# Optimization experiments

Hardware: AMD Instinct MI355X
Metric: run time of the kernel (lower is better)

## Reference

```python
import jax, jax.numpy as jnp
import numpy as np

B, T_DEC, S_ENC, D = 4, 128, 1024, 512
UNITS = 128


def setup_inputs() -> dict:
    key = jax.random.key(0)
    ks = jax.random.split(key, 5)
    dec = jax.random.normal(ks[0], (B, T_DEC, D), dtype=jnp.float32)
    enc = jax.random.normal(ks[1], (B, S_ENC, D), dtype=jnp.float32)
    # Glorot-ish scaled dense params
    W1 = jax.random.normal(ks[2], (D, UNITS), dtype=jnp.float32) / np.sqrt(D)
    b1 = jnp.zeros((UNITS,), dtype=jnp.float32)
    W2 = jax.random.normal(ks[3], (D, UNITS), dtype=jnp.float32) / np.sqrt(D)
    b2 = jnp.zeros((UNITS,), dtype=jnp.float32)
    v = jax.random.normal(ks[4], (UNITS,), dtype=jnp.float32) / np.sqrt(UNITS)
    v_b = jnp.zeros((1,), dtype=jnp.float32)
    return {"decoder_output": dec, "encoder_output": enc,
            "W1": W1, "b1": b1, "W2": W2, "b2": b2, "v": v, "v_b": v_b}


def reference(decoder_output, encoder_output, W1, b1, W2, b2, v, v_b):
    # Hoist the loop-invariant encoder projection (original recomputes it per step).
    w_enc = encoder_output @ W1 + b1            # [B, S, U]
    w_dec = decoder_output @ W2 + b2            # [B, T, U]
    # score[b,t,s] = v . tanh(w_enc[b,s] + w_dec[b,t]) + v_bias
    feat = jnp.tanh(w_enc[:, None, :, :] + w_dec[:, :, None, :])  # [B, T, S, U]
    scores = jnp.einsum('btsu,u->bts', feat, v) + v_b[0]          # [B, T, S]
    attention_weights = jax.nn.softmax(scores, axis=-1)           # [B, T, S]
    context_vector = jnp.einsum('bts,bsd->btd', attention_weights, encoder_output)
    return (context_vector, attention_weights)
```

## Files before the change

kernel.cpp:

```cpp
#include <hip/hip_runtime.h>
#include <math.h>

#define NB 4
#define TD 128
#define SE 1024
#define DD 512
#define UN 128
#define KSPLIT 4

__device__ __forceinline__ float exp2_raw(float x) {
  float r;
  asm("v_exp_f32 %0, %1" : "=v"(r) : "v"(x));
  return r;
}

__global__ __launch_bounds__(512, 2) void k_proj(const float* __restrict__ enc,
                                                 const float* __restrict__ dec,
                                                 const float* __restrict__ W1,
                                                 const float* __restrict__ b1,
                                                 const float* __restrict__ W2,
                                                 const float* __restrict__ b2,
                                                 float* __restrict__ wencT,
                                                 float* __restrict__ wdec) {
  __shared__ __align__(16) float At[16 * DD];
  __shared__ float red[KSPLIT][16][129];

  const int tx = threadIdx.x;
  const int rb = blockIdx.x;
  const bool is_enc = rb < 256;
  const int row_base = rb * 16;
  const float* __restrict__ src = is_enc
      ? (enc + (size_t)row_base * DD)
      : (dec + (size_t)(row_base - NB * SE) * DD);
  const float* __restrict__ W = is_enc ? W1 : W2;
  const float* __restrict__ bias = is_enc ? b1 : b2;
  const float K2 = 2.88539008f;

#pragma unroll
  for (int i = 0; i < 4; ++i) {
    const int idx = (i * 512 + tx) * 4;
    *(float4*)&At[idx] = *(const float4*)(src + idx);
  }
  __syncthreads();

  const int u2 = (tx & 63) * 2;
  const int wave = tx >> 6;
  const int ks = wave & 3;
  const int rh = wave >> 2;
  const int kb = ks * 128;
  const float* __restrict__ Wp = W + (size_t)kb * UN + u2;

  float acc[8][2] = {};
  for (int k = 0; k < 128; k += 4) {
    float4 a[8];
#pragma unroll
    for (int r = 0; r < 8; ++r)
      a[r] = *(const float4*)&At[(rh * 8 + r) * DD + kb + k];
#pragma unroll
    for (int j = 0; j < 4; ++j) {
      const float2 w = *(const float2*)(Wp + (size_t)(k + j) * UN);
#pragma unroll
      for (int r = 0; r < 8; ++r) {
        const float arj = ((const float*)&a[r])[j];
        acc[r][0] = fmaf(arj, w.x, acc[r][0]);
        acc[r][1] = fmaf(arj, w.y, acc[r][1]);
      }
    }
  }

#pragma unroll
  for (int r = 0; r < 8; ++r) {
    red[ks][rh * 8 + r][u2]     = acc[r][0];
    red[ks][rh * 8 + r][u2 + 1] = acc[r][1];
  }
  __syncthreads();

  const int u = tx >> 2;
  const int rq = (tx & 3) * 4;
  const float bu = bias[u];
  if (is_enc) {
    float o[4];
#pragma unroll
    for (int j = 0; j < 4; ++j) {
      const int row = rq + j;
      const float s = (red[0][row][u] + red[1][row][u]) +
                      (red[2][row][u] + red[3][row][u]);
      o[j] = exp2_raw(K2 * (s + bu));
    }
    const int b = row_base >> 10;
    const int s0 = row_base & 1023;
    *(float4*)(wencT + (size_t)(b * UN + u) * SE + s0 + rq) =
        make_float4(o[0], o[1], o[2], o[3]);
  } else {
    const int rb0 = row_base - NB * SE;
#pragma unroll
    for (int j = 0; j < 4; ++j) {
      const int row = rq + j;
      const float s = (red[0][row][u] + red[1][row][u]) +
                      (red[2][row][u] + red[3][row][u]);
      wdec[(size_t)(rb0 + row) * UN + u] = K2 * (s + bu);
    }
  }
}

__global__ __launch_bounds__(1024, 1) void k_score(const float* __restrict__ wdec,
                                                   const float* __restrict__ v,
                                                   const float* __restrict__ wencT,
                                                   float* __restrict__ attn) {
  __shared__ __align__(16) float wdE[2][UN];
  __shared__ __align__(16) float nv2[UN];
  __shared__ __align__(16) float parts[4][2][SE];
  __shared__ float redM[2][4], redS[2][4];

  const int wg = blockIdx.x;
  const int b = wg >> 6;
  const int t0 = (wg & 63) * 2;
  const int bt0 = b * TD + t0;
  const int tx = threadIdx.x;

  if (tx < 2 * UN) {
    const int tt = tx >> 7, u = tx & 127;
    wdE[tt][u] = exp2_raw(wdec[(size_t)(bt0 + tt) * UN + u]);
    if (tx < UN) nv2[tx] = -2.0f * v[tx];
  }
  __syncthreads();

  const int sq = tx & 255;
  const int uq = tx >> 8;
  const float* wp = wencT + (size_t)(b * UN + uq * 32) * SE + sq * 4;

  float a0[4] = {}, a1[4] = {};
#pragma unroll 2
  for (int ui4 = 0; ui4 < 32; ui4 += 4) {
    const int u0 = uq * 32 + ui4;
    const float4 nv = *(const float4*)&nv2[u0];
    const float4 E0v = *(const float4*)&wdE[0][u0];
    const float4 E1v = *(const float4*)&wdE[1][u0];
#pragma unroll
    for (int m = 0; m < 4; ++m) {
      const float4 ew = *(const float4*)(wp + (size_t)(ui4 + m) * SE);
      const float nvu = ((const float*)&nv)[m];
      const float E0 = ((const float*)&E0v)[m];
      const float E1 = ((const float*)&E1v)[m];
#pragma unroll
      for (int j = 0; j < 4; ++j) {
        const float e = ((const float*)&ew)[j];
        const float r0 = __builtin_amdgcn_rcpf(fmaf(e, E0, 1.0f));
        a0[j] = fmaf(nvu, r0, a0[j]);
        const float r1 = __builtin_amdgcn_rcpf(fmaf(e, E1, 1.0f));
        a1[j] = fmaf(nvu, r1, a1[j]);
      }
    }
  }
  *(float4*)&parts[uq][0][sq * 4] = make_float4(a0[0], a0[1], a0[2], a0[3]);
  *(float4*)&parts[uq][1][sq * 4] = make_float4(a1[0], a1[1], a1[2], a1[3]);
  __syncthreads();

  float sc[4], pv[4];
  const int tt = tx >> 8;
  const int q = tx & 255;
  if (tx < 512) {
    const float4 g0 = *(const float4*)&parts[0][tt][q * 4];
    const float4 g1 = *(const float4*)&parts[1][tt][q * 4];
    const float4 g2 = *(const float4*)&parts[2][tt][q * 4];
    const float4 g3 = *(const float4*)&parts[3][tt][q * 4];
    sc[0] = (g0.x + g1.x) + (g2.x + g3.x);
    sc[1] = (g0.y + g1.y) + (g2.y + g3.y);
    sc[2] = (g0.z + g1.z) + (g2.z + g3.z);
    sc[3] = (g0.w + g1.w) + (g2.w + g3.w);
    float m = fmaxf(fmaxf(sc[0], sc[1]), fmaxf(sc[2], sc[3]));
#pragma unroll
    for (int off = 32; off; off >>= 1) m = fmaxf(m, __shfl_xor(m, off));
    if ((tx & 63) == 0) redM[tt][(tx >> 6) & 3] = m;
  }
  __syncthreads();
  if (tx < 512) {
    const float m = fmaxf(fmaxf(redM[tt][0], redM[tt][1]),
                          fmaxf(redM[tt][2], redM[tt][3]));
    float s = 0.f;
#pragma unroll
    for (int j = 0; j < 4; ++j) { pv[j] = __expf(sc[j] - m); s += pv[j]; }
#pragma unroll
    for (int off = 32; off; off >>= 1) s += __shfl_xor(s, off);
    if ((tx & 63) == 0) redS[tt][(tx >> 6) & 3] = s;
  }
  __syncthreads();
  if (tx < 512) {
    const float s = (redS[tt][0] + redS[tt][1]) + (redS[tt][2] + redS[tt][3]);
    const float rinv = 1.0f / s;
    float* arow = attn + (size_t)(bt0 + tt) * SE + q * 4;
    *(float4*)arow = make_float4(pv[0] * rinv, pv[1] * rinv, pv[2] * rinv, pv[3] * rinv);
  }
}

__global__ __launch_bounds__(1024, 1) void k_ctx(const float* __restrict__ attn,
                                                 const float* __restrict__ enc,
                                                 float* __restrict__ ctx) {
  __shared__ __align__(16) float at[8][SE];
  __shared__ __align__(16) float red[16][8][128];

  const int wg = blockIdx.x;
  const int dt = wg & 3;
  const int tg = (wg >> 2) & 15;
  const int b = wg >> 6;
  const int tx = threadIdx.x;

#pragma unroll
  for (int i = 0; i < 2; ++i) {
    const int idx = i * 1024 + tx;
    const int row = idx >> 8;
    const int c = (idx & 255) * 4;
    *(float4*)&at[row][c] =
        *(const float4*)(attn + (size_t)(b * TD + tg * 8 + row) * SE + c);
  }
  __syncthreads();

  const int w = tx >> 6;
  const int dp = (tx & 63) * 2;
  const int sbeg = w * 64;
  const float* ep = enc + ((size_t)b * SE + sbeg) * DD + dt * 128 + dp;

  float2 acc[8] = {};
  for (int s = 0; s < 64; s += 4) {
    float4 av[8];
#pragma unroll
    for (int t = 0; t < 8; ++t)
      av[t] = *(const float4*)&at[t][sbeg + s];
#pragma unroll
    for (int j = 0; j < 4; ++j) {
      const float2 ev = *(const float2*)(ep + (size_t)(s + j) * DD);
#pragma unroll
      for (int t = 0; t < 8; ++t) {
        const float a = ((const float*)&av[t])[j];
        acc[t].x = fmaf(a, ev.x, acc[t].x);
        acc[t].y = fmaf(a, ev.y, acc[t].y);
      }
    }
  }
#pragma unroll
  for (int t = 0; t < 8; ++t)
    *(float2*)&red[w][t][dp] = acc[t];
  __syncthreads();

  const int t = tx >> 7;
  const int d = tx & 127;
  float o = 0.f;
#pragma unroll
  for (int q = 0; q < 16; ++q) o += red[q][t][d];
  ctx[(size_t)(b * TD + tg * 8 + t) * DD + dt * 128 + d] = o;
}

extern "C" void kernel_launch(void* const* d_in, const int* in_sizes, int n_in,
                              void* d_out, int out_size, void* d_ws, size_t ws_size,
                              hipStream_t stream) {
  const float* dec = (const float*)d_in[0];
  const float* enc = (const float*)d_in[1];
  const float* W1  = (const float*)d_in[2];
  const float* b1  = (const float*)d_in[3];
  const float* W2  = (const float*)d_in[4];
  const float* b2  = (const float*)d_in[5];
  const float* v   = (const float*)d_in[6];

  float* ctx  = (float*)d_out;
  float* attn = (float*)d_out + (size_t)NB * TD * DD;

  float* ws    = (float*)d_ws;
  float* wencT = ws;
  float* wdec  = wencT + (size_t)NB * UN * SE;

  hipLaunchKernelGGL(k_proj, dim3(288), dim3(512), 0, stream,
                     enc, dec, W1, b1, W2, b2, wencT, wdec);
  hipLaunchKernelGGL(k_score, dim3(256), dim3(1024), 0, stream,
                     wdec, v, wencT, attn);
  hipLaunchKernelGGL(k_ctx, dim3(256), dim3(1024), 0, stream, attn, enc, ctx);
}
```

Measured before the change: 45.25 us.

## Reduce score partials across lanes with shuffles instead of shared memory

```diff
diff --git a/kernel.cpp b/kernel.cpp
--- a/kernel.cpp
+++ b/kernel.cpp
@@ -107,10 +107,9 @@
                                                    const float* __restrict__ v,
                                                    const float* __restrict__ wencT,
                                                    float* __restrict__ attn) {
-  __shared__ __align__(16) float wdE[2][UN];
-  __shared__ __align__(16) float nv2[UN];
-  __shared__ __align__(16) float parts[4][2][SE];
-  __shared__ float redM[2][4], redS[2][4];
+  __shared__ __align__(16) float wdEr[2][4][132];
+  __shared__ __align__(16) float nv2r[4][132];
+  __shared__ float redM[2][16], redS[2][16];
 
   const int wg = blockIdx.x;
   const int b = wg >> 6;
@@ -120,22 +119,28 @@
 
   if (tx < 2 * UN) {
     const int tt = tx >> 7, u = tx & 127;
-    wdE[tt][u] = exp2_raw(wdec[(size_t)(bt0 + tt) * UN + u]);
-    if (tx < UN) nv2[tx] = -2.0f * v[tx];
-  }
-  __syncthreads();
-
-  const int sq = tx & 255;
-  const int uq = tx >> 8;
+    const float e = exp2_raw(wdec[(size_t)(bt0 + tt) * UN + u]);
+#pragma unroll
+    for (int c = 0; c < 4; ++c) wdEr[tt][c][u] = e;
+    if (tx < UN) {
+      const float nv = -2.0f * v[tx];
+#pragma unroll
+      for (int c = 0; c < 4; ++c) nv2r[c][tx] = nv;
+    }
+  }
+  __syncthreads();
+
+  const int sq = tx >> 2;
+  const int uq = tx & 3;
   const float* wp = wencT + (size_t)(b * UN + uq * 32) * SE + sq * 4;
 
   float a0[4] = {}, a1[4] = {};
 #pragma unroll 2
   for (int ui4 = 0; ui4 < 32; ui4 += 4) {
     const int u0 = uq * 32 + ui4;
-    const float4 nv = *(const float4*)&nv2[u0];
-    const float4 E0v = *(const float4*)&wdE[0][u0];
-    const float4 E1v = *(const float4*)&wdE[1][u0];
+    const float4 nv = *(const float4*)&nv2r[uq][u0];
+    const float4 E0v = *(const float4*)&wdEr[0][uq][u0];
+    const float4 E1v = *(const float4*)&wdEr[1][uq][u0];
 #pragma unroll
     for (int m = 0; m < 4; ++m) {
       const float4 ew = *(const float4*)(wp + (size_t)(ui4 + m) * SE);
@@ -152,44 +157,56 @@
       }
     }
   }
-  *(float4*)&parts[uq][0][sq * 4] = make_float4(a0[0], a0[1], a0[2], a0[3]);
-  *(float4*)&parts[uq][1][sq * 4] = make_float4(a1[0], a1[1], a1[2], a1[3]);
-  __syncthreads();
-
-  float sc[4], pv[4];
-  const int tt = tx >> 8;
-  const int q = tx & 255;
-  if (tx < 512) {
-    const float4 g0 = *(const float4*)&parts[0][tt][q * 4];
-    const float4 g1 = *(const float4*)&parts[1][tt][q * 4];
-    const float4 g2 = *(const float4*)&parts[2][tt][q * 4];
-    const float4 g3 = *(const float4*)&parts[3][tt][q * 4];
-    sc[0] = (g0.x + g1.x) + (g2.x + g3.x);
-    sc[1] = (g0.y + g1.y) + (g2.y + g3.y);
-    sc[2] = (g0.z + g1.z) + (g2.z + g3.z);
-    sc[3] = (g0.w + g1.w) + (g2.w + g3.w);
-    float m = fmaxf(fmaxf(sc[0], sc[1]), fmaxf(sc[2], sc[3]));
-#pragma unroll
-    for (int off = 32; off; off >>= 1) m = fmaxf(m, __shfl_xor(m, off));
-    if ((tx & 63) == 0) redM[tt][(tx >> 6) & 3] = m;
-  }
-  __syncthreads();
-  if (tx < 512) {
-    const float m = fmaxf(fmaxf(redM[tt][0], redM[tt][1]),
-                          fmaxf(redM[tt][2], redM[tt][3]));
-    float s = 0.f;
-#pragma unroll
-    for (int j = 0; j < 4; ++j) { pv[j] = __expf(sc[j] - m); s += pv[j]; }
-#pragma unroll
-    for (int off = 32; off; off >>= 1) s += __shfl_xor(s, off);
-    if ((tx & 63) == 0) redS[tt][(tx >> 6) & 3] = s;
-  }
-  __syncthreads();
-  if (tx < 512) {
-    const float s = (redS[tt][0] + redS[tt][1]) + (redS[tt][2] + redS[tt][3]);
-    const float rinv = 1.0f / s;
-    float* arow = attn + (size_t)(bt0 + tt) * SE + q * 4;
-    *(float4*)arow = make_float4(pv[0] * rinv, pv[1] * rinv, pv[2] * rinv, pv[3] * rinv);
+
+#pragma unroll
+  for (int j = 0; j < 4; ++j) {
+    a0[j] += __shfl_xor(a0[j], 1); a0[j] += __shfl_xor(a0[j], 2);
+    a1[j] += __shfl_xor(a1[j], 1); a1[j] += __shfl_xor(a1[j], 2);
+  }
+
+  float m0 = fmaxf(fmaxf(a0[0], a0[1]), fmaxf(a0[2], a0[3]));
+  float m1 = fmaxf(fmaxf(a1[0], a1[1]), fmaxf(a1[2], a1[3]));
+#pragma unroll
+  for (int off = 4; off <= 32; off <<= 1) {
+    m0 = fmaxf(m0, __shfl_xor(m0, off));
+    m1 = fmaxf(m1, __shfl_xor(m1, off));
+  }
+  const int wv = tx >> 6;
+  if ((tx & 63) == 0) { redM[0][wv] = m0; redM[1][wv] = m1; }
+  __syncthreads();
+  m0 = redM[0][0]; m1 = redM[1][0];
+#pragma unroll
+  for (int q = 1; q < 16; ++q) {
+    m0 = fmaxf(m0, redM[0][q]);
+    m1 = fmaxf(m1, redM[1][q]);
+  }
+
+  float p0[4], p1[4];
+  float s0 = 0.f, s1 = 0.f;
+#pragma unroll
+  for (int j = 0; j < 4; ++j) {
+    p0[j] = __expf(a0[j] - m0); s0 += p0[j];
+    p1[j] = __expf(a1[j] - m1); s1 += p1[j];
+  }
+#pragma unroll
+  for (int off = 4; off <= 32; off <<= 1) {
+    s0 += __shfl_xor(s0, off);
+    s1 += __shfl_xor(s1, off);
+  }
+  if ((tx & 63) == 0) { redS[0][wv] = s0; redS[1][wv] = s1; }
+  __syncthreads();
+  s0 = 0.f; s1 = 0.f;
+#pragma unroll
+  for (int q = 0; q < 16; ++q) { s0 += redS[0][q]; s1 += redS[1][q]; }
+  const float r0 = 1.0f / s0;
+  const float r1 = 1.0f / s1;
+
+  if (uq == 0) {
+    float* arow0 = attn + (size_t)bt0 * SE + sq * 4;
+    *(float4*)arow0 =
+        make_float4(p0[0] * r0, p0[1] * r0, p0[2] * r0, p0[3] * r0);
+    *(float4*)(arow0 + SE) =
+        make_float4(p1[0] * r1, p1[1] * r1, p1[2] * r1, p1[3] * r1);
   }
 }
 
```

New measurement: 52.14 us. 1.15x slower.

## Restructure score kernel to one decoder step per 512-thread block

Applied to the files above, without the earlier changes.

```diff
diff --git a/kernel.cpp b/kernel.cpp
--- a/kernel.cpp
+++ b/kernel.cpp
@@ -103,93 +103,82 @@
   }
 }
 
-__global__ __launch_bounds__(1024, 1) void k_score(const float* __restrict__ wdec,
-                                                   const float* __restrict__ v,
-                                                   const float* __restrict__ wencT,
-                                                   float* __restrict__ attn) {
-  __shared__ __align__(16) float wdE[2][UN];
+__global__ __launch_bounds__(512, 2) void k_score(const float* __restrict__ wdec,
+                                                  const float* __restrict__ v,
+                                                  const float* __restrict__ wencT,
+                                                  float* __restrict__ attn) {
+  __shared__ __align__(16) float wdE[UN];
   __shared__ __align__(16) float nv2[UN];
-  __shared__ __align__(16) float parts[4][2][SE];
-  __shared__ float redM[2][4], redS[2][4];
+  __shared__ __align__(16) float parts[2][SE];
+  __shared__ float redM[4], redS[4];
 
   const int wg = blockIdx.x;
-  const int b = wg >> 6;
-  const int t0 = (wg & 63) * 2;
-  const int bt0 = b * TD + t0;
+  const int b = wg >> 7;
+  const int t = wg & 127;
+  const int bt = b * TD + t;
   const int tx = threadIdx.x;
 
-  if (tx < 2 * UN) {
-    const int tt = tx >> 7, u = tx & 127;
-    wdE[tt][u] = exp2_raw(wdec[(size_t)(bt0 + tt) * UN + u]);
-    if (tx < UN) nv2[tx] = -2.0f * v[tx];
+  if (tx < UN) {
+    wdE[tx] = exp2_raw(wdec[(size_t)bt * UN + tx]);
+    nv2[tx] = -2.0f * v[tx];
   }
   __syncthreads();
 
   const int sq = tx & 255;
-  const int uq = tx >> 8;
-  const float* wp = wencT + (size_t)(b * UN + uq * 32) * SE + sq * 4;
-
-  float a0[4] = {}, a1[4] = {};
+  const int uh = tx >> 8;
+  const float* wp = wencT + (size_t)(b * UN + uh * 64) * SE + sq * 4;
+
+  float a0[4] = {};
 #pragma unroll 2
-  for (int ui4 = 0; ui4 < 32; ui4 += 4) {
-    const int u0 = uq * 32 + ui4;
+  for (int ui4 = 0; ui4 < 64; ui4 += 4) {
+    const int u0 = uh * 64 + ui4;
     const float4 nv = *(const float4*)&nv2[u0];
-    const float4 E0v = *(const float4*)&wdE[0][u0];
-    const float4 E1v = *(const float4*)&wdE[1][u0];
+    const float4 Ev = *(const float4*)&wdE[u0];
 #pragma unroll
     for (int m = 0; m < 4; ++m) {
       const float4 ew = *(const float4*)(wp + (size_t)(ui4 + m) * SE);
       const float nvu = ((const float*)&nv)[m];
-      const float E0 = ((const float*)&E0v)[m];
-      const float E1 = ((const float*)&E1v)[m];
+      const float E0 = ((const float*)&Ev)[m];
 #pragma unroll
       for (int j = 0; j < 4; ++j) {
         const float e = ((const float*)&ew)[j];
         const float r0 = __builtin_amdgcn_rcpf(fmaf(e, E0, 1.0f));
         a0[j] = fmaf(nvu, r0, a0[j]);
-        const float r1 = __builtin_amdgcn_rcpf(fmaf(e, E1, 1.0f));
-        a1[j] = fmaf(nvu, r1, a1[j]);
       }
     }
   }
-  *(float4*)&parts[uq][0][sq * 4] = make_float4(a0[0], a0[1], a0[2], a0[3]);
-  *(float4*)&parts[uq][1][sq * 4] = make_float4(a1[0], a1[1], a1[2], a1[3]);
+  *(float4*)&parts[uh][sq * 4] = make_float4(a0[0], a0[1], a0[2], a0[3]);
   __syncthreads();
 
   float sc[4], pv[4];
-  const int tt = tx >> 8;
   const int q = tx & 255;
-  if (tx < 512) {
-    const float4 g0 = *(const float4*)&parts[0][tt][q * 4];
-    const float4 g1 = *(const float4*)&parts[1][tt][q * 4];
-    const float4 g2 = *(const float4*)&parts[2][tt][q * 4];
-    const float4 g3 = *(const float4*)&parts[3][tt][q * 4];
-    sc[0] = (g0.x + g1.x) + (g2.x + g3.x);
-    sc[1] = (g0.y + g1.y) + (g2.y + g3.y);
-    sc[2] = (g0.z + g1.z) + (g2.z + g3.z);
-    sc[3] = (g0.w + g1.w) + (g2.w + g3.w);
+  if (tx < 256) {
+    const float4 g0 = *(const float4*)&parts[0][q * 4];
+    const float4 g1 = *(const float4*)&parts[1][q * 4];
+    sc[0] = g0.x + g1.x; sc[1] = g0.y + g1.y;
+    sc[2] = g0.z + g1.z; sc[3] = g0.w + g1.w;
     float m = fmaxf(fmaxf(sc[0], sc[1]), fmaxf(sc[2], sc[3]));
 #pragma unroll
     for (int off = 32; off; off >>= 1) m = fmaxf(m, __shfl_xor(m, off));
-    if ((tx & 63) == 0) redM[tt][(tx >> 6) & 3] = m;
-  }
-  __syncthreads();
-  if (tx < 512) {
-    const float m = fmaxf(fmaxf(redM[tt][0], redM[tt][1]),
-                          fmaxf(redM[tt][2], redM[tt][3]));
+    if ((tx & 63) == 0) redM[tx >> 6] = m;
+  }
+  __syncthreads();
+  if (tx < 256) {
+    const float m = fmaxf(fmaxf(redM[0], redM[1]), fmaxf(redM[2], redM[3]));
     float s = 0.f;
 #pragma unroll
     for (int j = 0; j < 4; ++j) { pv[j] = __expf(sc[j] - m); s += pv[j]; }
 #pragma unroll
     for (int off = 32; off; off >>= 1) s += __shfl_xor(s, off);
-    if ((tx & 63) == 0) redS[tt][(tx >> 6) & 3] = s;
-  }
-  __syncthreads();
-  if (tx < 512) {
-    const float s = (redS[tt][0] + redS[tt][1]) + (redS[tt][2] + redS[tt][3]);
+    if ((tx & 63) == 0) redS[tx >> 6] = s;
+  }
+  __syncthreads();
+  if (tx < 256) {
+    const float s = (redS[0] + redS[1]) + (redS[2] + redS[3]);
     const float rinv = 1.0f / s;
-    float* arow = attn + (size_t)(bt0 + tt) * SE + q * 4;
-    *(float4*)arow = make_float4(pv[0] * rinv, pv[1] * rinv, pv[2] * rinv, pv[3] * rinv);
+    float* arow = attn + (size_t)bt * SE + q * 4;
+    *(float4*)arow = make_float4(pv[0] * rinv, pv[1] * rinv,
+                                 pv[2] * rinv, pv[3] * rinv);
   }
 }
 
@@ -270,7 +259,7 @@
 
   hipLaunchKernelGGL(k_proj, dim3(288), dim3(512), 0, stream,
                      enc, dec, W1, b1, W2, b2, wencT, wdec);
-  hipLaunchKernelGGL(k_score, dim3(256), dim3(1024), 0, stream,
+  hipLaunchKernelGGL(k_score, dim3(512), dim3(512), 0, stream,
                      wdec, v, wencT, attn);
   hipLaunchKernelGGL(k_ctx, dim3(256), dim3(1024), 0, stream, attn, enc, ctx);
 }
```

Result: slower. 47.83 us (+5.7%).
